# Kernel optimization log

Measured on AMD Instinct MI355X. Metric: run time of the kernel, lower is better.

Reference implementation:

```python
import jax, jax.numpy as jnp
import numpy as np
import math

B, CK, T, H, W = 4, 64, 8, 30, 54
N, CV = 8, 512

def setup_inputs() -> dict:
    key = jax.random.key(0)
    k1, k2, k3, k4 = jax.random.split(key, 4)
    mem_keys = jax.random.normal(k1, (B, CK, T, H, W), dtype=jnp.float32)
    mem_values = jax.random.normal(k2, (N, CV, T, H, W), dtype=jnp.float32)
    qk = jax.random.normal(k3, (B, CK, H, W), dtype=jnp.float32)
    broadcast_map = jax.random.randint(k4, (N,), 0, B, dtype=jnp.int64)
    return {"mem_keys": mem_keys, "mem_values": mem_values, "qk": qk,
            "broadcast_map": broadcast_map}

def reference(mem_keys, mem_values, qk, broadcast_map):
    # STCNModel.read_memory
    Bq, CKq, Tq, Hq, Wq = mem_keys.shape
    mk = mem_keys.reshape(Bq, CKq, Tq * Hq * Wq)      # [B, CK, THW]
    q = qk.reshape(Bq, CKq, Hq * Wq)                   # [B, CK, HW]
    a_sq = jnp.sum(mk * mk, axis=1)[:, :, None]        # [B, THW, 1]
    ab = jnp.einsum('bct,bcq->btq', mk, q)             # [B, THW, HW]
    frame_affinity = (2.0 * ab - a_sq) / math.sqrt(CKq)
    # softmax over memory dim (axis=1)
    frame_affinity = jax.nn.softmax(frame_affinity, axis=1)
    obj_affinity = frame_affinity[broadcast_map]       # [N, THW, HW]
    Nn, CVv = mem_values.shape[0], mem_values.shape[1]
    mo = mem_values.reshape(Nn, CVv, Tq * Hq * Wq)     # [N, CV, THW]
    obj_read = jnp.einsum('nct,ntq->ncq', mo, obj_affinity)
    return obj_read.reshape(Nn, CVv, Hq, Wq)
```

## Files before the change

### kernel.cpp

```cpp
#include <hip/hip_runtime.h>
#include <hip/hip_bf16.h>

#define CKDIM 64
#define THW   12960
#define HWDIM 1620
#define NOBJ  8
#define CVAL  512
#define NB    4
#define NSTEP 405
#define NJT   13
#define NCHS  8
#define NCHP  4
#define PCH   16
#define S2F   0.3606737602222409f

#if defined(__has_builtin)
#if __has_builtin(__builtin_amdgcn_global_load_lds)
#define HAVE_GLL 1
#endif
#endif

using bf16x8 = __attribute__((ext_vector_type(8))) short;
using f32x4  = __attribute__((ext_vector_type(4))) float;

__device__ __forceinline__ unsigned cvtpk(float lo, float hi) {
    unsigned r;
    asm("v_cvt_pk_bf16_f32 %0, %1, %2" : "=v"(r) : "v"(lo), "v"(hi));
    return r;
}
__device__ __forceinline__ unsigned short bf_rne(float x) {
    unsigned u = __float_as_uint(x);
    u += 0x7FFFu + ((u >> 16) & 1u);
    return (unsigned short)(u >> 16);
}
__device__ __forceinline__ float fexp2(float x) {
#if __has_builtin(__builtin_amdgcn_exp2f)
    return __builtin_amdgcn_exp2f(x);
#else
    return __expf(x * 0.69314718055994531f);
#endif
}
#ifdef HAVE_GLL
__device__ __forceinline__ void gload16(const void* g, void* l) {
    __builtin_amdgcn_global_load_lds(
        (const __attribute__((address_space(1))) unsigned int*)g,
        (__attribute__((address_space(3))) unsigned int*)l, 16, 0, 0);
}
#endif

__global__ void stcn_ksq_kernel(const float* __restrict__ mk, float* __restrict__ k8l) {
    int t = blockIdx.x * 256 + threadIdx.x;
    if (t >= THW) return;
    int b = blockIdx.y;
    const float* p = mk + (size_t)b * CKDIM * THW + t;
    float s = 0.f;
#pragma unroll
    for (int c = 0; c < CKDIM; ++c) { float v = p[(size_t)c * THW]; s = fmaf(v, v, s); }
    k8l[b * THW + t] = s * (0.125f * 1.44269504088896341f);
}

__global__ __launch_bounds__(512)
void stcn_ktr_kernel(const float* __restrict__ mk, unsigned short* __restrict__ kbt) {
    __shared__ unsigned short L[64][72];
    const int tid = threadIdx.x, b = blockIdx.y, t0 = blockIdx.x * 64;
#pragma unroll
    for (int it = 0; it < 8; ++it) {
        int idx = tid + 512 * it;
        int tt = idx & 63, c = idx >> 6;
        int t = t0 + tt;
        float v = (t < THW) ? mk[((size_t)b * CKDIM + c) * THW + t] : 0.f;
        L[tt][c] = bf_rne(v);
    }
    __syncthreads();
    int tt = tid >> 3, cq = tid & 7;
    int t = t0 + tt;
    if (t < THW) {
        uint4 o = *(const uint4*)&L[tt][8 * cq];
        *(uint4*)(kbt + ((size_t)b * THW + t) * CKDIM + 8 * cq) = o;
    }
}

__global__ void stcn_vcvt_kernel(const float* __restrict__ mv, unsigned short* __restrict__ mvb) {
    size_t i = ((size_t)blockIdx.x * 256 + threadIdx.x) * 8;
    if (i >= (size_t)NOBJ * CVAL * THW) return;
    float4 v0 = *(const float4*)(mv + i);
    float4 v1 = *(const float4*)(mv + i + 4);
    uint4 o;
    o.x = cvtpk(v0.x, v0.y); o.y = cvtpk(v0.z, v0.w);
    o.z = cvtpk(v1.x, v1.y); o.w = cvtpk(v1.z, v1.w);
    *(uint4*)(mvb + i) = o;
}

template <int MODE, bool VB16, bool KB16>
__global__ __launch_bounds__(512, (MODE == 1) ? 4 : 1)
void stcn_aff_kernel(const float* __restrict__ mk, const unsigned short* __restrict__ kbt,
                     const float* __restrict__ qk, const float* __restrict__ k8l,
                     float* __restrict__ mpart, float* __restrict__ lpart,
                     const float* __restrict__ mv, const unsigned short* __restrict__ mvb,
                     const int* __restrict__ bmap, float* __restrict__ out)
{
    constexpr int SMEM_BYTES = (MODE == 0) ? 36864 : 45312;
    __shared__ __align__(16) unsigned char smem[SMEM_BYTES];
    unsigned short* KtP   = (unsigned short*)smem;
    float*          k8tP  = (float*)(smem + 9216);
    unsigned short* PtP   = (unsigned short*)(smem + 9472);
    unsigned short* VtP   = (unsigned short*)(smem + 23808);
    float*          mjsP  = (float*)(smem + 44288);
    float*          iljsP = (float*)(smem + 44800);
    unsigned short* QtP   = (unsigned short*)smem;

    const int tid  = threadIdx.x;
    const int w    = tid >> 6;
    const int lane = tid & 63;
    const int g    = lane >> 4;
    const int lr   = lane & 15;

    int b, n = 0, jt, kc, cb = 0;
    if (MODE == 0) { b = blockIdx.y; jt = blockIdx.x >> 3; kc = blockIdx.x & 7; }
    else {
        n = blockIdx.y; jt = blockIdx.x >> 3; kc = (blockIdx.x >> 1) & 3; cb = blockIdx.x & 1;
        b = bmap[n];
    }
    const int jbase = jt * 128;
    const int cbase = cb * 256;

#pragma unroll
    for (int it = 0; it < 8; ++it) {
        int idx = tid + 512 * it;
        int j = idx & 127, cp = idx >> 7;
        int jg = jbase + j;
        float q0 = 0.f, q1 = 0.f;
        if (jg < HWDIM) {
            const float* qp = qk + ((size_t)b * CKDIM + 2 * cp) * HWDIM + jg;
            q0 = qp[0]; q1 = qp[HWDIM];
        }
        unsigned wh = cvtpk(q0, q1);
        float r0 = q0 - __uint_as_float(wh << 16);
        float r1 = q1 - __uint_as_float(wh & 0xFFFF0000u);
        *(unsigned*)&QtP[(0 * 128 + j) * 72 + 2 * cp] = wh;
        *(unsigned*)&QtP[(1 * 128 + j) * 72 + 2 * cp] = cvtpk(r0, r1);
    }
    __syncthreads();
    bf16x8 bqh[2], bql[2];
#pragma unroll
    for (int s = 0; s < 2; ++s) {
        bqh[s] = *(const bf16x8*)&QtP[(0 * 128 + w * 16 + lr) * 72 + 32 * s + 8 * g];
        bql[s] = *(const bf16x8*)&QtP[(1 * 128 + w * 16 + lr) * 72 + 32 * s + 8 * g];
    }
    __syncthreads();

    auto stageK_loads = [&](int st, uint2& k16, float2* kvf) {
        if constexpr (KB16) {
            int tt = tid >> 4, cq = tid & 15;
            k16 = *(const uint2*)(kbt + ((size_t)b * THW + st * 32 + tt) * CKDIM + 4 * cq);
        } else {
#pragma unroll
            for (int it = 0; it < 2; ++it) {
                int idx = tid + 512 * it;
                int tt = idx & 31, cp = idx >> 5;
                const float* kp = mk + ((size_t)b * CKDIM + 2 * cp) * THW + st * 32 + tt;
                kvf[it].x = kp[0];
                kvf[it].y = kp[THW];
            }
        }
    };
    auto stageK_write = [&](int buf, uint2 k16, const float2* kvf) {
        if constexpr (KB16) {
            int tt = tid >> 4, cq = tid & 15;
            *(uint2*)&KtP[(buf * 32 + tt) * 72 + 4 * cq] = k16;
        } else {
#pragma unroll
            for (int it = 0; it < 2; ++it) {
                int idx = tid + 512 * it;
                int tt = idx & 31, cp = idx >> 5;
                *(unsigned*)&KtP[(buf * 32 + tt) * 72 + 2 * cp] = cvtpk(kvf[it].x, kvf[it].y);
            }
        }
    };

    int s0, s1;
    if (MODE == 0) { s0 = (NSTEP * kc) / NCHS; s1 = (NSTEP * (kc + 1)) / NCHS; }
    else           { s0 = (NSTEP * kc) / NCHP; s1 = (NSTEP * (kc + 1)) / NCHP; }

    if (MODE == 1 && tid < 128) {
        int jg = jbase + tid;
        float m = 0.f, l = 0.f;
        if (jg < HWDIM) {
            m = -1e30f;
#pragma unroll
            for (int c = 0; c < NCHS; ++c) {
                float mc = mpart[(b * NCHS + c) * HWDIM + jg];
                float lc = lpart[(b * NCHS + c) * HWDIM + jg];
                float mn = fmaxf(m, mc);
                l = l * fexp2(m - mn) + lc * fexp2(mc - mn);
                m = mn;
            }
        }
        mjsP[tid]  = m;
        iljsP[tid] = (l > 0.f) ? 1.f / l : 0.f;
    }
    {
        uint2 k16; float2 kvf[2];
        stageK_loads(s0, k16, kvf);
        stageK_write(0, k16, kvf);
        if (tid < 32) k8tP[tid] = k8l[b * THW + s0 * 32 + tid];
    }
    __syncthreads();

    float mv_j = 0.f, il_j = 0.f;
    if (MODE == 1) { mv_j = mjsP[w * 16 + lr]; il_j = iljsP[w * 16 + lr]; }

    float m_run = -1e30f, l_run = 0.f;
    f32x4 zz = {0.f, 0.f, 0.f, 0.f};
    f32x4 acc[4][4];
    if (MODE == 1)
#pragma unroll
        for (int i = 0; i < 4; ++i)
#pragma unroll
            for (int j = 0; j < 4; ++j) acc[i][j] = zz;

    const int wc = w >> 1, wj = w & 1;
    const int vc = tid >> 1, vth = tid & 1;

    int cur = 0;
    for (int st = s0; st < s1; ++st) {
        const int t0 = st * 32;
        const bool nxt = (st + 1 < s1);

        uint4 vw0 = {0,0,0,0}, vw1 = {0,0,0,0};
        if (MODE == 1) {
            if (VB16) {
                const unsigned short* vp = mvb + ((size_t)n * CVAL + cbase + vc) * THW + t0 + vth * 16;
                vw0 = *(const uint4*)vp;
                vw1 = *(const uint4*)(vp + 8);
            } else {
                const float* vp = mv + ((size_t)n * CVAL + cbase + vc) * THW + t0 + vth * 16;
                float4 f0 = *(const float4*)vp;
                float4 f1 = *(const float4*)(vp + 4);
                float4 f2 = *(const float4*)(vp + 8);
                float4 f3 = *(const float4*)(vp + 12);
                vw0 = make_uint4(cvtpk(f0.x,f0.y), cvtpk(f0.z,f0.w), cvtpk(f1.x,f1.y), cvtpk(f1.z,f1.w));
                vw1 = make_uint4(cvtpk(f2.x,f2.y), cvtpk(f2.z,f2.w), cvtpk(f3.x,f3.y), cvtpk(f3.z,f3.w));
            }
        }
        uint2 k16; float2 kvf[2];
        float k8next = 0.f;
        if (nxt) {
            stageK_loads(st + 1, k16, kvf);
            if (tid < 32) k8next = k8l[b * THW + (st + 1) * 32 + tid];
        }
        bf16x8 ak0[2], ak1[2];
#pragma unroll
        for (int s = 0; s < 2; ++s) {
            ak0[s] = *(const bf16x8*)&KtP[(cur * 32 + lr) * 72 + 32 * s + 8 * g];
            ak1[s] = *(const bf16x8*)&KtP[(cur * 32 + 16 + lr) * 72 + 32 * s + 8 * g];
        }
        f32x4 k80 = *(const f32x4*)&k8tP[cur * 32 + 4 * g];
        f32x4 k81 = *(const f32x4*)&k8tP[cur * 32 + 16 + 4 * g];
        f32x4 ab0 = zz, ab1 = zz;
#pragma unroll
        for (int s = 0; s < 2; ++s) {
            ab0 = __builtin_amdgcn_mfma_f32_16x16x32_bf16(ak0[s], bqh[s], ab0, 0, 0, 0);
            ab0 = __builtin_amdgcn_mfma_f32_16x16x32_bf16(ak0[s], bql[s], ab0, 0, 0, 0);
            ab1 = __builtin_amdgcn_mfma_f32_16x16x32_bf16(ak1[s], bqh[s], ab1, 0, 0, 0);
            ab1 = __builtin_amdgcn_mfma_f32_16x16x32_bf16(ak1[s], bql[s], ab1, 0, 0, 0);
        }
        if (nxt) {
            stageK_write(cur ^ 1, k16, kvf);
            if (tid < 32) k8tP[(cur ^ 1) * 32 + tid] = k8next;
        }

        if (MODE == 0) {
            float L0[4], L1[4], tmax = -1e30f;
#pragma unroll
            for (int r = 0; r < 4; ++r) {
                L0[r] = fmaf(ab0[r], S2F, -k80[r]); tmax = fmaxf(tmax, L0[r]);
                L1[r] = fmaf(ab1[r], S2F, -k81[r]); tmax = fmaxf(tmax, L1[r]);
            }
            float ps = 0.f;
#pragma unroll
            for (int r = 0; r < 4; ++r)
                ps += fexp2(L0[r] - tmax) + fexp2(L1[r] - tmax);
            float mn = fmaxf(m_run, tmax);
            l_run = l_run * fexp2(m_run - mn) + ps * fexp2(tmax - mn);
            m_run = mn;
            __syncthreads();
        } else {
            float p0[4], p1[4];
#pragma unroll
            for (int r = 0; r < 4; ++r) {
                p0[r] = fexp2(fmaf(ab0[r], S2F, -k80[r]) - mv_j) * il_j;
                p1[r] = fexp2(fmaf(ab1[r], S2F, -k81[r]) - mv_j) * il_j;
            }
            __syncthreads();
            {
                int jl = w * 16 + lr;
                *(uint2*)&PtP[jl * 56 + 4 * g]      = make_uint2(cvtpk(p0[0], p0[1]), cvtpk(p0[2], p0[3]));
                *(uint2*)&PtP[jl * 56 + 16 + 4 * g] = make_uint2(cvtpk(p1[0], p1[1]), cvtpk(p1[2], p1[3]));
                *(uint4*)&VtP[vc * 40 + vth * 16]     = vw0;
                *(uint4*)&VtP[vc * 40 + vth * 16 + 8] = vw1;
            }
            __syncthreads();
            bf16x8 bp[4];
#pragma unroll
            for (int jf = 0; jf < 4; ++jf)
                bp[jf] = *(const bf16x8*)&PtP[(wj * 64 + jf * 16 + lr) * 56 + 8 * g];
#pragma unroll
            for (int cf = 0; cf < 4; ++cf) {
                bf16x8 av = *(const bf16x8*)&VtP[(wc * 64 + cf * 16 + lr) * 40 + 8 * g];
#pragma unroll
                for (int jf = 0; jf < 4; ++jf)
                    acc[cf][jf] = __builtin_amdgcn_mfma_f32_16x16x32_bf16(av, bp[jf], acc[cf][jf], 0, 0, 0);
            }
        }
        cur ^= 1;
    }

    if (MODE == 0) {
#pragma unroll
        for (int off = 16; off < 64; off <<= 1) {
            float mo = __shfl_xor(m_run, off, 64);
            float lo = __shfl_xor(l_run, off, 64);
            float mn = fmaxf(m_run, mo);
            l_run = l_run * fexp2(m_run - mn) + lo * fexp2(mo - mn);
            m_run = mn;
        }
        int jg = jbase + w * 16 + lr;
        if (g == 0 && jg < HWDIM) {
            mpart[(b * NCHS + kc) * HWDIM + jg] = m_run;
            lpart[(b * NCHS + kc) * HWDIM + jg] = l_run;
        }
    } else {
#pragma unroll
        for (int cf = 0; cf < 4; ++cf) {
#pragma unroll
            for (int jf = 0; jf < 4; ++jf) {
                int jg = jbase + wj * 64 + jf * 16 + lr;
                if (jg < HWDIM) {
                    int c = cbase + wc * 64 + cf * 16 + 4 * g;
                    float* op = out + ((size_t)n * CVAL + c) * HWDIM + jg;
#pragma unroll
                    for (int r = 0; r < 4; ++r)
                        atomicAdd(op + (size_t)r * HWDIM, acc[cf][jf][r]);
                }
            }
        }
    }
}

__global__ __launch_bounds__(512)
void stcn_pwrite_kernel(const unsigned short* __restrict__ kbt,
                        const float* __restrict__ qk, const float* __restrict__ k8l,
                        const float* __restrict__ mpart, const float* __restrict__ lpart,
                        unsigned short* __restrict__ Pws, int bbase)
{
    __shared__ __align__(16) unsigned char smem[36864];
    unsigned short* KtP   = (unsigned short*)smem;
    float*          k8tP  = (float*)(smem + 9216);
    unsigned short* PtP   = (unsigned short*)(smem + 9472);
    float*          mjsP  = (float*)(smem + 23808);
    float*          iljsP = (float*)(smem + 24320);
    unsigned short* QtP   = (unsigned short*)smem;

    const int tid  = threadIdx.x;
    const int w    = tid >> 6;
    const int lane = tid & 63;
    const int g    = lane >> 4;
    const int lr   = lane & 15;

    const int bb = blockIdx.y;
    const int b  = bbase + bb;
    const int jt = blockIdx.x >> 4, kc = blockIdx.x & 15;
    const int jbase = jt * 128;

#pragma unroll
    for (int it = 0; it < 8; ++it) {
        int idx = tid + 512 * it;
        int j = idx & 127, cp = idx >> 7;
        int jg = jbase + j;
        float q0 = 0.f, q1 = 0.f;
        if (jg < HWDIM) {
            const float* qp = qk + ((size_t)b * CKDIM + 2 * cp) * HWDIM + jg;
            q0 = qp[0]; q1 = qp[HWDIM];
        }
        unsigned wh = cvtpk(q0, q1);
        float r0 = q0 - __uint_as_float(wh << 16);
        float r1 = q1 - __uint_as_float(wh & 0xFFFF0000u);
        *(unsigned*)&QtP[(0 * 128 + j) * 72 + 2 * cp] = wh;
        *(unsigned*)&QtP[(1 * 128 + j) * 72 + 2 * cp] = cvtpk(r0, r1);
    }
    __syncthreads();
    bf16x8 bqh[2], bql[2];
#pragma unroll
    for (int s = 0; s < 2; ++s) {
        bqh[s] = *(const bf16x8*)&QtP[(0 * 128 + w * 16 + lr) * 72 + 32 * s + 8 * g];
        bql[s] = *(const bf16x8*)&QtP[(1 * 128 + w * 16 + lr) * 72 + 32 * s + 8 * g];
    }
    __syncthreads();

    const int s0 = (NSTEP * kc) / PCH, s1 = (NSTEP * (kc + 1)) / PCH;

    if (tid < 128) {
        int jg = jbase + tid;
        float m = 0.f, l = 0.f;
        if (jg < HWDIM) {
            m = -1e30f;
#pragma unroll
            for (int c = 0; c < NCHS; ++c) {
                float mc = mpart[(b * NCHS + c) * HWDIM + jg];
                float lc = lpart[(b * NCHS + c) * HWDIM + jg];
                float mn = fmaxf(m, mc);
                l = l * fexp2(m - mn) + lc * fexp2(mc - mn);
                m = mn;
            }
        }
        mjsP[tid]  = m;
        iljsP[tid] = (l > 0.f) ? 1.f / l : 0.f;
    }
    {
        int tt = tid >> 4, cq = tid & 15;
        uint2 k16 = *(const uint2*)(kbt + ((size_t)b * THW + s0 * 32 + tt) * CKDIM + 4 * cq);
        *(uint2*)&KtP[tt * 72 + 4 * cq] = k16;
        if (tid < 32) k8tP[tid] = k8l[b * THW + s0 * 32 + tid];
    }
    __syncthreads();

    const float mv_j = mjsP[w * 16 + lr], il_j = iljsP[w * 16 + lr];
    f32x4 zz = {0.f, 0.f, 0.f, 0.f};

    int cur = 0;
    for (int st = s0; st < s1; ++st) {
        const int t0 = st * 32;
        const bool nxt = (st + 1 < s1);
        uint2 k16;
        float k8next = 0.f;
        const int tt = tid >> 4, cq = tid & 15;
        if (nxt) {
            k16 = *(const uint2*)(kbt + ((size_t)b * THW + (st + 1) * 32 + tt) * CKDIM + 4 * cq);
            if (tid < 32) k8next = k8l[b * THW + (st + 1) * 32 + tid];
        }
        bf16x8 ak0[2], ak1[2];
#pragma unroll
        for (int s = 0; s < 2; ++s) {
            ak0[s] = *(const bf16x8*)&KtP[(cur * 32 + lr) * 72 + 32 * s + 8 * g];
            ak1[s] = *(const bf16x8*)&KtP[(cur * 32 + 16 + lr) * 72 + 32 * s + 8 * g];
        }
        f32x4 k80 = *(const f32x4*)&k8tP[cur * 32 + 4 * g];
        f32x4 k81 = *(const f32x4*)&k8tP[cur * 32 + 16 + 4 * g];
        f32x4 ab0 = zz, ab1 = zz;
#pragma unroll
        for (int s = 0; s < 2; ++s) {
            ab0 = __builtin_amdgcn_mfma_f32_16x16x32_bf16(ak0[s], bqh[s], ab0, 0, 0, 0);
            ab0 = __builtin_amdgcn_mfma_f32_16x16x32_bf16(ak0[s], bql[s], ab0, 0, 0, 0);
            ab1 = __builtin_amdgcn_mfma_f32_16x16x32_bf16(ak1[s], bqh[s], ab1, 0, 0, 0);
            ab1 = __builtin_amdgcn_mfma_f32_16x16x32_bf16(ak1[s], bql[s], ab1, 0, 0, 0);
        }
        if (nxt) {
            *(uint2*)&KtP[((cur ^ 1) * 32 + tt) * 72 + 4 * cq] = k16;
            if (tid < 32) k8tP[(cur ^ 1) * 32 + tid] = k8next;
        }
        float p0[4], p1[4];
#pragma unroll
        for (int r = 0; r < 4; ++r) {
            p0[r] = fexp2(fmaf(ab0[r], S2F, -k80[r]) - mv_j) * il_j;
            p1[r] = fexp2(fmaf(ab1[r], S2F, -k81[r]) - mv_j) * il_j;
        }
        __syncthreads();
        {
            int jl = w * 16 + lr;
            *(uint2*)&PtP[jl * 56 + 4 * g]      = make_uint2(cvtpk(p0[0], p0[1]), cvtpk(p0[2], p0[3]));
            *(uint2*)&PtP[jl * 56 + 16 + 4 * g] = make_uint2(cvtpk(p1[0], p1[1]), cvtpk(p1[2], p1[3]));
        }
        __syncthreads();
        {
            int jr = tid >> 2, qq = tid & 3;
            int jg = jbase + jr;
            if (jg < HWDIM)
                *(uint4*)(Pws + ((size_t)bb * HWDIM + jg) * THW + t0 + qq * 8) =
                    *(const uint4*)&PtP[jr * 56 + qq * 8];
        }
        cur ^= 1;
    }
}

template <bool FULLP>
__global__ __launch_bounds__(256, 4)
void stcn_gemm3_kernel(const unsigned short* __restrict__ mvb,
                       const unsigned short* __restrict__ Pws,
                       const int* __restrict__ bmap, float* __restrict__ out, int phase)
{
    __shared__ __align__(16) unsigned short Av[2][128 * 32];
    __shared__ __align__(16) unsigned short Bv[2][128 * 32];

    const int n = blockIdx.y;
    const int b = bmap[n];
    int bslot;
    if constexpr (FULLP) { bslot = b; }
    else { if ((b >> 1) != phase) return; bslot = b & 1; }

    const int x    = blockIdx.x;
    const int ks   = x & 1;
    const int rest = x >> 1;
    const int jn   = rest % NJT;
    const int cm   = rest / NJT;
    const int jbase = jn * 128, cbase = cm * 128;

    const int tid = threadIdx.x;
    const int w = tid >> 6, lane = tid & 63, g = lane >> 4, lr = lane & 15;
    const int wc = w >> 1, wj = w & 1;

    const int srow = tid >> 2;
    const int tsw  = (((tid & 3) ^ ((tid >> 3) & 3)) << 3);
    const int gs8  = ((g ^ ((lr >> 1) & 3)) << 3);

    const int s0 = (NSTEP * ks) / 2, s1 = (NSTEP * (ks + 1)) / 2;

    const unsigned short* abase = mvb + ((size_t)n * CVAL + cbase) * THW;
    const unsigned short* bbase = Pws + (size_t)bslot * HWDIM * THW;
    int jr0 = jbase + srow;       if (jr0 >= HWDIM) jr0 = 0;
    int jr1 = jbase + 64 + srow;  if (jr1 >= HWDIM) jr1 = 0;
    const unsigned short* ga0 = abase + (size_t)(srow) * THW + tsw;
    const unsigned short* ga1 = abase + (size_t)(64 + srow) * THW + tsw;
    const unsigned short* gb0 = bbase + (size_t)jr0 * THW + tsw;
    const unsigned short* gb1 = bbase + (size_t)jr1 * THW + tsw;

    f32x4 zz = {0.f, 0.f, 0.f, 0.f};
    f32x4 acc[4][4];
#pragma unroll
    for (int i = 0; i < 4; ++i)
#pragma unroll
        for (int j = 0; j < 4; ++j) acc[i][j] = zz;

#ifdef HAVE_GLL
    auto stage = [&](int buf, int st) {
        const int t0 = st * 32;
        gload16(ga0 + t0, &Av[buf][0    + w * 512]);
        gload16(ga1 + t0, &Av[buf][2048 + w * 512]);
        gload16(gb0 + t0, &Bv[buf][0    + w * 512]);
        gload16(gb1 + t0, &Bv[buf][2048 + w * 512]);
    };
    stage(0, s0);
#else
    {
        const int t0 = s0 * 32;
        *(uint4*)&Av[0][tid * 8]        = *(const uint4*)(ga0 + t0);
        *(uint4*)&Av[0][2048 + tid * 8] = *(const uint4*)(ga1 + t0);
        *(uint4*)&Bv[0][tid * 8]        = *(const uint4*)(gb0 + t0);
        *(uint4*)&Bv[0][2048 + tid * 8] = *(const uint4*)(gb1 + t0);
    }
#endif
    __syncthreads();

    int cur = 0;
    for (int st = s0; st < s1; ++st) {
        const bool nxt = (st + 1 < s1);
#ifdef HAVE_GLL
        if (nxt) stage(cur ^ 1, st + 1);
#else
        uint4 ra0, ra1, rb0, rb1;
        if (nxt) {
            const int t0 = (st + 1) * 32;
            ra0 = *(const uint4*)(ga0 + t0);
            ra1 = *(const uint4*)(ga1 + t0);
            rb0 = *(const uint4*)(gb0 + t0);
            rb1 = *(const uint4*)(gb1 + t0);
        }
#endif
        bf16x8 av[4], bp[4];
#pragma unroll
        for (int cf = 0; cf < 4; ++cf)
            av[cf] = *(const bf16x8*)&Av[cur][(wc * 64 + cf * 16 + lr) * 32 + gs8];
#pragma unroll
        for (int jf = 0; jf < 4; ++jf)
            bp[jf] = *(const bf16x8*)&Bv[cur][(wj * 64 + jf * 16 + lr) * 32 + gs8];
#pragma unroll
        for (int cf = 0; cf < 4; ++cf)
#pragma unroll
            for (int jf = 0; jf < 4; ++jf)
                acc[cf][jf] = __builtin_amdgcn_mfma_f32_16x16x32_bf16(av[cf], bp[jf], acc[cf][jf], 0, 0, 0);
#ifndef HAVE_GLL
        if (nxt) {
            *(uint4*)&Av[cur ^ 1][tid * 8]        = ra0;
            *(uint4*)&Av[cur ^ 1][2048 + tid * 8] = ra1;
            *(uint4*)&Bv[cur ^ 1][tid * 8]        = rb0;
            *(uint4*)&Bv[cur ^ 1][2048 + tid * 8] = rb1;
        }
#endif
        __syncthreads();
        cur ^= 1;
    }

#pragma unroll
    for (int cf = 0; cf < 4; ++cf)
#pragma unroll
        for (int jf = 0; jf < 4; ++jf) {
            int jg = jbase + wj * 64 + jf * 16 + lr;
            if (jg < HWDIM) {
                int c = cbase + wc * 64 + cf * 16 + 4 * g;
                float* op = out + ((size_t)n * CVAL + c) * HWDIM + jg;
#pragma unroll
                for (int r = 0; r < 4; ++r)
                    atomicAdd(op + (size_t)r * HWDIM, acc[cf][jf][r]);
            }
        }
}

extern "C" void kernel_launch(void* const* d_in, const int* in_sizes, int n_in,
                              void* d_out, int out_size, void* d_ws, size_t ws_size,
                              hipStream_t stream) {
    (void)in_sizes; (void)n_in;
    const float* mk   = (const float*)d_in[0];
    const float* mv   = (const float*)d_in[1];
    const float* qkp  = (const float*)d_in[2];
    const int*   bmap = (const int*)d_in[3];
    float* out = (float*)d_out;

    float* k8l   = (float*)d_ws;
    float* mpart = k8l + NB * THW;
    float* lpart = mpart + NB * NCHS * HWDIM;
    unsigned short* mvb = (unsigned short*)(lpart + NB * NCHS * HWDIM);
    unsigned short* kbt = mvb + (size_t)NOBJ * CVAL * THW;
    unsigned short* Pws = kbt + (size_t)NB * THW * CKDIM;

    size_t base_bytes = (size_t)(NB * THW + 2 * NB * NCHS * HWDIM) * 4;
    size_t need_vb  = base_bytes + (size_t)NOBJ * CVAL * THW * 2;
    size_t need_kbt = need_vb + (size_t)NB * THW * CKDIM * 2;
    size_t need_P2  = need_kbt + (size_t)2 * HWDIM * THW * 2;
    size_t need_P4  = need_kbt + (size_t)4 * HWDIM * THW * 2;
    bool use_vb16 = (ws_size >= need_vb);
    bool use_kbt  = (ws_size >= need_kbt);
    bool use_P2   = (ws_size >= need_P2);
    bool use_P4   = (ws_size >= need_P4);

    hipMemsetAsync(d_out, 0, (size_t)out_size * sizeof(float), stream);
    stcn_ksq_kernel<<<dim3((THW + 255) / 256, NB), 256, 0, stream>>>(mk, k8l);
    if (use_kbt)
        stcn_ktr_kernel<<<dim3((THW + 63) / 64, NB), 512, 0, stream>>>(mk, kbt);
    if (use_vb16) {
        size_t nthreads = (size_t)NOBJ * CVAL * THW / 8;
        stcn_vcvt_kernel<<<(unsigned)((nthreads + 255) / 256), 256, 0, stream>>>(mv, mvb);
    }

    if (use_kbt)
        stcn_aff_kernel<0, false, true><<<dim3(NJT * NCHS, NB), 512, 0, stream>>>(
            mk, kbt, qkp, k8l, mpart, lpart, nullptr, nullptr, nullptr, nullptr);
    else
        stcn_aff_kernel<0, false, false><<<dim3(NJT * NCHS, NB), 512, 0, stream>>>(
            mk, nullptr, qkp, k8l, mpart, lpart, nullptr, nullptr, nullptr, nullptr);

    if (use_P4 && use_kbt) {
        stcn_pwrite_kernel<<<dim3(NJT * PCH, NB), 512, 0, stream>>>(
            kbt, qkp, k8l, mpart, lpart, Pws, 0);
        stcn_gemm3_kernel<true><<<dim3(104, NOBJ), 256, 0, stream>>>(
            mvb, Pws, bmap, out, 0);
    } else if (use_P2 && use_kbt) {
        for (int p = 0; p < 2; ++p) {
            stcn_pwrite_kernel<<<dim3(NJT * PCH, 2), 512, 0, stream>>>(
                kbt, qkp, k8l, mpart, lpart, Pws, 2 * p);
            stcn_gemm3_kernel<false><<<dim3(104, NOBJ), 256, 0, stream>>>(
                mvb, Pws, bmap, out, p);
        }
    } else {
        dim3 g1(NJT * NCHP * 2, NOBJ);
        if (use_vb16 && use_kbt)
            stcn_aff_kernel<1, true, true><<<g1, 512, 0, stream>>>(
                mk, kbt, qkp, k8l, mpart, lpart, nullptr, mvb, bmap, out);
        else if (use_vb16)
            stcn_aff_kernel<1, true, false><<<g1, 512, 0, stream>>>(
                mk, nullptr, qkp, k8l, mpart, lpart, nullptr, mvb, bmap, out);
        else
            stcn_aff_kernel<1, false, false><<<g1, 512, 0, stream>>>(
                mk, nullptr, qkp, k8l, mpart, lpart, mv, nullptr, bmap, out);
    }
}
```

Before: 553.2 us.

## Fuse key-norm into transpose kernel and split GEMM3 K four ways with XCD-aware mapping

The squared-norm computation of memory keys moves into the bf16 transpose kernel, so mem_keys is read once and one launch disappears. The final value GEMM in the full-P path now uses a 1D grid of 1664 workgroups with a 4-way K split instead of 2-way. Block IDs are remapped so consecutive workgroups on the same XCD share an object and channel tile, which should improve L2 reuse. The added split doubles the atomic accumulation traffic into the output.

```diff
diff --git a/kernel.cpp b/kernel.cpp
--- a/kernel.cpp
+++ b/kernel.cpp
@@ -60,23 +60,38 @@
 }
 
 __global__ __launch_bounds__(512)
-void stcn_ktr_kernel(const float* __restrict__ mk, unsigned short* __restrict__ kbt) {
+void stcn_ktr_kernel(const float* __restrict__ mk, unsigned short* __restrict__ kbt,
+                     float* __restrict__ k8l) {
     __shared__ unsigned short L[64][72];
+    __shared__ float S[64][8];
     const int tid = threadIdx.x, b = blockIdx.y, t0 = blockIdx.x * 64;
+    const int tt = tid & 63;
+    float a2 = 0.f;
 #pragma unroll
     for (int it = 0; it < 8; ++it) {
         int idx = tid + 512 * it;
-        int tt = idx & 63, c = idx >> 6;
+        int c = idx >> 6;
         int t = t0 + tt;
         float v = (t < THW) ? mk[((size_t)b * CKDIM + c) * THW + t] : 0.f;
         L[tt][c] = bf_rne(v);
-    }
+        a2 = fmaf(v, v, a2);
+    }
+    S[tt][tid >> 6] = a2;
     __syncthreads();
-    int tt = tid >> 3, cq = tid & 7;
-    int t = t0 + tt;
-    if (t < THW) {
-        uint4 o = *(const uint4*)&L[tt][8 * cq];
-        *(uint4*)(kbt + ((size_t)b * THW + t) * CKDIM + 8 * cq) = o;
+    if (tid < 64) {
+        float s = 0.f;
+#pragma unroll
+        for (int q = 0; q < 8; ++q) s += S[tid][q];
+        int t = t0 + tid;
+        if (t < THW) k8l[b * THW + t] = s * (0.125f * 1.44269504088896341f);
+    }
+    {
+        int tr = tid >> 3, cq = tid & 7;
+        int t = t0 + tr;
+        if (t < THW) {
+            uint4 o = *(const uint4*)&L[tr][8 * cq];
+            *(uint4*)(kbt + ((size_t)b * THW + t) * CKDIM + 8 * cq) = o;
+        }
     }
 }
 
@@ -492,17 +507,31 @@
     __shared__ __align__(16) unsigned short Av[2][128 * 32];
     __shared__ __align__(16) unsigned short Bv[2][128 * 32];
 
-    const int n = blockIdx.y;
+    int n, cm, jn, ks, ksplit;
+    if constexpr (FULLP) {
+        int wg  = blockIdx.x;
+        int vid = (wg & 7) * 208 + (wg >> 3);
+        n = vid / 208;
+        int r  = vid % 208;
+        cm = r / 52;
+        int r2 = r % 52;
+        jn = r2 >> 2;
+        ks = r2 & 3;
+        ksplit = 4;
+    } else {
+        n = blockIdx.y;
+        const int x = blockIdx.x;
+        ks = x & 1;
+        const int rest = x >> 1;
+        jn = rest % NJT;
+        cm = rest / NJT;
+        ksplit = 2;
+    }
     const int b = bmap[n];
     int bslot;
     if constexpr (FULLP) { bslot = b; }
     else { if ((b >> 1) != phase) return; bslot = b & 1; }
 
-    const int x    = blockIdx.x;
-    const int ks   = x & 1;
-    const int rest = x >> 1;
-    const int jn   = rest % NJT;
-    const int cm   = rest / NJT;
     const int jbase = jn * 128, cbase = cm * 128;
 
     const int tid = threadIdx.x;
@@ -513,7 +542,7 @@
     const int tsw  = (((tid & 3) ^ ((tid >> 3) & 3)) << 3);
     const int gs8  = ((g ^ ((lr >> 1) & 3)) << 3);
 
-    const int s0 = (NSTEP * ks) / 2, s1 = (NSTEP * (ks + 1)) / 2;
+    const int s0 = (NSTEP * ks) / ksplit, s1 = (NSTEP * (ks + 1)) / ksplit;
 
     const unsigned short* abase = mvb + ((size_t)n * CVAL + cbase) * THW;
     const unsigned short* bbase = Pws + (size_t)bslot * HWDIM * THW;
@@ -633,9 +662,10 @@
     bool use_P4   = (ws_size >= need_P4);
 
     hipMemsetAsync(d_out, 0, (size_t)out_size * sizeof(float), stream);
-    stcn_ksq_kernel<<<dim3((THW + 255) / 256, NB), 256, 0, stream>>>(mk, k8l);
     if (use_kbt)
-        stcn_ktr_kernel<<<dim3((THW + 63) / 64, NB), 512, 0, stream>>>(mk, kbt);
+        stcn_ktr_kernel<<<dim3((THW + 63) / 64, NB), 512, 0, stream>>>(mk, kbt, k8l);
+    else
+        stcn_ksq_kernel<<<dim3((THW + 255) / 256, NB), 256, 0, stream>>>(mk, k8l);
     if (use_vb16) {
         size_t nthreads = (size_t)NOBJ * CVAL * THW / 8;
         stcn_vcvt_kernel<<<(unsigned)((nthreads + 255) / 256), 256, 0, stream>>>(mv, mvb);
@@ -651,7 +681,7 @@
     if (use_P4 && use_kbt) {
         stcn_pwrite_kernel<<<dim3(NJT * PCH, NB), 512, 0, stream>>>(
             kbt, qkp, k8l, mpart, lpart, Pws, 0);
-        stcn_gemm3_kernel<true><<<dim3(104, NOBJ), 256, 0, stream>>>(
+        stcn_gemm3_kernel<true><<<dim3(1664), 256, 0, stream>>>(
             mvb, Pws, bmap, out, 0);
     } else if (use_P2 && use_kbt) {
         for (int p = 0; p < 2; ++p) {
```

New measurement: 526.0 us. -4.9%, faster.
